# Optimization experiments

Hardware: AMD Instinct MI355X
Metric: run time of the kernel (lower is better)

The kernel has to match this reference:

```python
import jax, jax.numpy as jnp
import numpy as np

N_NODES = 10000
IN_CH = 128
OUT_CH = 128
N_EDGES = 320000


def setup_inputs() -> dict:
    key = jax.random.key(0)
    k1, k2, k3, k4 = jax.random.split(key, 4)
    x = jax.random.normal(k1, (N_NODES, IN_CH), dtype=jnp.float32)
    edge_index = jax.random.randint(k2, (N_EDGES, 2), 0, N_NODES, dtype=jnp.int64)
    # Linear weights (torch stores [out, in]); scale like kaiming-uniform-ish
    w = jax.random.normal(k3, (OUT_CH, IN_CH), dtype=jnp.float32) / np.sqrt(IN_CH)
    b = jax.random.normal(k4, (OUT_CH, IN_CH), dtype=jnp.float32) / np.sqrt(IN_CH)
    return {"x": x, "edge_index": edge_index, "w": w, "b": b}


def reference(x, edge_index, w, b):
    n = x.shape[0]
    # Each edge (i, j) contributes x[j] to node i and x[i] to node j (undirected).
    src = jnp.concatenate([edge_index[:, 1], edge_index[:, 0]])  # feature source
    dst = jnp.concatenate([edge_index[:, 0], edge_index[:, 1]])  # aggregation target
    # segment-sum of gathered neighbor features -> [n, in_ch]
    agg_sum = jax.ops.segment_sum(x[src], dst, num_segments=n)
    deg = jax.ops.segment_sum(jnp.ones_like(dst, dtype=x.dtype), dst, num_segments=n)
    # mean with zero fallback for isolated nodes (original uses zeros vector)
    agg = jnp.where(deg[:, None] > 0, agg_sum / jnp.maximum(deg, 1.0)[:, None], 0.0)
    # out = ReLU(agg @ w^T + x @ b^T)
    return jax.nn.relu(agg @ w.T + x @ b.T)
```

## Files before the change

kernel.cpp:

```cpp
#include <hip/hip_runtime.h>

#define N_NODES 10000
#define CH 128
#define N_EDGES 320000
#define CAP 128
#define CSTR 16


__device__ __forceinline__ unsigned short f2bf(float f) {
    unsigned u = __float_as_uint(f);
    return (unsigned short)((u + 0x7FFFu + ((u >> 16) & 1u)) >> 16);
}
__device__ __forceinline__ float bf2f(unsigned short h) {
    return __uint_as_float(((unsigned)h) << 16);
}

__global__ __launch_bounds__(256) void fill_kernel(const int* __restrict__ ei,
                                                   int* __restrict__ cursor,
                                                   unsigned short* __restrict__ adj)
{
    const int t = blockIdx.x * blockDim.x + threadIdx.x;
    if (t >= N_EDGES) return;
    const int2 p = ((const int2*)ei)[t];
    if ((unsigned)p.x >= N_NODES || (unsigned)p.y >= N_NODES) return;
    const int s0 = atomicAdd(&cursor[p.x * CSTR], 1);
    const int s1 = atomicAdd(&cursor[p.y * CSTR], 1);
    if (s0 < CAP) adj[(size_t)p.x * CAP + s0] = (unsigned short)p.y;
    if (s1 < CAP) adj[(size_t)p.y * CAP + s1] = (unsigned short)p.x;
}

__global__ __launch_bounds__(256) void gather_kernel(const float* __restrict__ x,
                                                     const int* __restrict__ cursor,
                                                     const unsigned short* __restrict__ adj,
                                                     unsigned short* __restrict__ aggb)
{
    const int wv   = threadIdx.x >> 6;
    const int node = blockIdx.x * 4 + wv;
    const int lane = threadIdx.x & 63;
    const int h    = lane >> 5;
    const int l    = lane & 31;

    const int deg = cursor[node * CSTR];
    const int d   = deg < CAP ? deg : CAP;
    const unsigned short* nb = adj + (size_t)node * CAP;

    float4 acc = {0.f, 0.f, 0.f, 0.f};
    const int nit = (d + 1) >> 1;
#pragma unroll 4
    for (int it = 0; it < nit; ++it) {
        const int idx = 2 * it + h;
        int j = nb[idx];
        j = j < N_NODES ? j : 0;
        const float4 u = ((const float4*)(x + (size_t)j * CH))[l];
        const float m = idx < d ? 1.0f : 0.0f;
        acc.x += m * u.x; acc.y += m * u.y; acc.z += m * u.z; acc.w += m * u.w;
    }
    acc.x += __shfl_xor(acc.x, 32, 64);
    acc.y += __shfl_xor(acc.y, 32, 64);
    acc.z += __shfl_xor(acc.z, 32, 64);
    acc.w += __shfl_xor(acc.w, 32, 64);

    if (h == 0) {
        const float inv = deg > 0 ? 1.0f / (float)deg : 0.0f;
        ushort4 o;
        o.x = f2bf(acc.x * inv);
        o.y = f2bf(acc.y * inv);
        o.z = f2bf(acc.z * inv);
        o.w = f2bf(acc.w * inv);
        ((ushort4*)(aggb + (size_t)node * CH))[l] = o;
    }
}

#define NPB 16
__global__ __launch_bounds__(256) void gemm_relu_kernel(const unsigned short* __restrict__ aggb,
                                                        const float* __restrict__ x,
                                                        const float* __restrict__ w,
                                                        const float* __restrict__ b,
                                                        float* __restrict__ out)
{
    __shared__ float sh_a[NPB * CH];
    __shared__ float sh_x[NPB * CH];
    const int tid   = threadIdx.x;
    const int node0 = blockIdx.x * NPB;

    const ushort4* ag = (const ushort4*)(aggb + (size_t)node0 * CH);
#pragma unroll
    for (int r = 0; r < 2; ++r) {
        const ushort4 q = ag[tid + r * 256];
        const int base = (tid + r * 256) * 4;
        sh_a[base + 0] = bf2f(q.x);
        sh_a[base + 1] = bf2f(q.y);
        sh_a[base + 2] = bf2f(q.z);
        sh_a[base + 3] = bf2f(q.w);
    }
    ((float4*)sh_x)[tid]       = ((const float4*)(x + (size_t)node0 * CH))[tid];
    ((float4*)sh_x)[tid + 256] = ((const float4*)(x + (size_t)node0 * CH))[tid + 256];
    __syncthreads();

    const int o = tid & 127;
    const int g = tid >> 7;
    const float4* wr = (const float4*)(w + (size_t)o * CH);
    const float4* br = (const float4*)(b + (size_t)o * CH);
    const float4* A  = (const float4*)(sh_a + (size_t)(g * 8) * CH);
    const float4* X  = (const float4*)(sh_x + (size_t)(g * 8) * CH);

    float acc[8] = {0.f, 0.f, 0.f, 0.f, 0.f, 0.f, 0.f, 0.f};
#pragma unroll 4
    for (int k = 0; k < CH / 4; ++k) {
        const float4 wv = wr[k];
        const float4 bv = br[k];
#pragma unroll
        for (int n = 0; n < 8; ++n) {
            const float4 a4 = A[n * (CH / 4) + k];
            const float4 x4 = X[n * (CH / 4) + k];
            acc[n] += a4.x * wv.x + a4.y * wv.y + a4.z * wv.z + a4.w * wv.w
                    + x4.x * bv.x + x4.y * bv.y + x4.z * bv.z + x4.w * bv.w;
        }
    }
#pragma unroll
    for (int n = 0; n < 8; ++n) {
        const int node = node0 + g * 8 + n;
        const float v = acc[n];
        out[(size_t)node * CH + o] = v > 0.f ? v : 0.f;
    }
}

extern "C" void kernel_launch(void* const* d_in, const int* in_sizes, int n_in,
                              void* d_out, int out_size, void* d_ws, size_t ws_size,
                              hipStream_t stream)
{
    const float* x  = (const float*)d_in[0];
    const int*   ei = (const int*)d_in[1];
    const float* w  = (const float*)d_in[2];
    const float* b  = (const float*)d_in[3];
    float*       out = (float*)d_out;

    int*            cursor = (int*)d_ws;
    unsigned short* adj    = (unsigned short*)((char*)d_ws + 640000);
    unsigned short* aggb   = (unsigned short*)((char*)d_ws + 3200000);

    hipMemsetAsync(d_ws, 0, (size_t)N_NODES * CSTR * sizeof(int), stream);

    fill_kernel<<<(N_EDGES + 255) / 256, 256, 0, stream>>>(ei, cursor, adj);
    gather_kernel<<<N_NODES / 4, 256, 0, stream>>>(x, cursor, adj, aggb);
    gemm_relu_kernel<<<N_NODES / NPB, 256, 0, stream>>>(aggb, x, w, b, out);
}
```

Before: 140.6 us.

## Fuse gather into GEMM, gather bf16 copy of x, merge conversion into fill

The neighbor gather-mean moves into the GEMM kernel, so the aggregate goes straight to shared memory and the bf16 aggregate round-trip through global memory and one launch disappear. Neighbor features are now read from a bf16 copy of x, which halves gather traffic. That copy is built by extra blocks in the same launch as the adjacency fill. In exchange, the fused kernel has only 625 blocks, each doing 16 serial-ish gathers, which may hurt occupancy and latency hiding, and the input features are rounded to bf16 before summation.

```diff
diff --git a/kernel.cpp b/kernel.cpp
--- a/kernel.cpp
+++ b/kernel.cpp
@@ -5,6 +5,11 @@
 #define N_EDGES 320000
 #define CAP 128
 #define CSTR 16
+
+#define FILL_BLOCKS ((N_EDGES + 255) / 256)
+#define CONV_THREADS (N_NODES * CH / 8)
+#define CONV_BLOCKS ((CONV_THREADS + 255) / 256)
+#define NPB 16
 
 
 __device__ __forceinline__ unsigned short f2bf(float f) {
@@ -15,86 +20,93 @@
     return __uint_as_float(((unsigned)h) << 16);
 }
 
-__global__ __launch_bounds__(256) void fill_kernel(const int* __restrict__ ei,
-                                                   int* __restrict__ cursor,
-                                                   unsigned short* __restrict__ adj)
+__global__ __launch_bounds__(256) void fill_conv_kernel(const int* __restrict__ ei,
+                                                        int* __restrict__ cursor,
+                                                        unsigned short* __restrict__ adj,
+                                                        const float* __restrict__ x,
+                                                        unsigned short* __restrict__ xb)
 {
-    const int t = blockIdx.x * blockDim.x + threadIdx.x;
-    if (t >= N_EDGES) return;
-    const int2 p = ((const int2*)ei)[t];
-    if ((unsigned)p.x >= N_NODES || (unsigned)p.y >= N_NODES) return;
-    const int s0 = atomicAdd(&cursor[p.x * CSTR], 1);
-    const int s1 = atomicAdd(&cursor[p.y * CSTR], 1);
-    if (s0 < CAP) adj[(size_t)p.x * CAP + s0] = (unsigned short)p.y;
-    if (s1 < CAP) adj[(size_t)p.y * CAP + s1] = (unsigned short)p.x;
-}
-
-__global__ __launch_bounds__(256) void gather_kernel(const float* __restrict__ x,
-                                                     const int* __restrict__ cursor,
-                                                     const unsigned short* __restrict__ adj,
-                                                     unsigned short* __restrict__ aggb)
-{
-    const int wv   = threadIdx.x >> 6;
-    const int node = blockIdx.x * 4 + wv;
-    const int lane = threadIdx.x & 63;
-    const int h    = lane >> 5;
-    const int l    = lane & 31;
-
-    const int deg = cursor[node * CSTR];
-    const int d   = deg < CAP ? deg : CAP;
-    const unsigned short* nb = adj + (size_t)node * CAP;
-
-    float4 acc = {0.f, 0.f, 0.f, 0.f};
-    const int nit = (d + 1) >> 1;
-#pragma unroll 4
-    for (int it = 0; it < nit; ++it) {
-        const int idx = 2 * it + h;
-        int j = nb[idx];
-        j = j < N_NODES ? j : 0;
-        const float4 u = ((const float4*)(x + (size_t)j * CH))[l];
-        const float m = idx < d ? 1.0f : 0.0f;
-        acc.x += m * u.x; acc.y += m * u.y; acc.z += m * u.z; acc.w += m * u.w;
-    }
-    acc.x += __shfl_xor(acc.x, 32, 64);
-    acc.y += __shfl_xor(acc.y, 32, 64);
-    acc.z += __shfl_xor(acc.z, 32, 64);
-    acc.w += __shfl_xor(acc.w, 32, 64);
-
-    if (h == 0) {
-        const float inv = deg > 0 ? 1.0f / (float)deg : 0.0f;
-        ushort4 o;
-        o.x = f2bf(acc.x * inv);
-        o.y = f2bf(acc.y * inv);
-        o.z = f2bf(acc.z * inv);
-        o.w = f2bf(acc.w * inv);
-        ((ushort4*)(aggb + (size_t)node * CH))[l] = o;
+    const int bid = blockIdx.x;
+    if (bid < FILL_BLOCKS) {
+        const int t = bid * 256 + threadIdx.x;
+        if (t >= N_EDGES) return;
+        const int2 p = ((const int2*)ei)[t];
+        if ((unsigned)p.x >= N_NODES || (unsigned)p.y >= N_NODES) return;
+        const int s0 = atomicAdd(&cursor[p.x * CSTR], 1);
+        const int s1 = atomicAdd(&cursor[p.y * CSTR], 1);
+        if (s0 < CAP) adj[(size_t)p.x * CAP + s0] = (unsigned short)p.y;
+        if (s1 < CAP) adj[(size_t)p.y * CAP + s1] = (unsigned short)p.x;
+    } else {
+        const int t = (bid - FILL_BLOCKS) * 256 + threadIdx.x;
+        if (t >= CONV_THREADS) return;
+        const float4 a = ((const float4*)x)[t * 2];
+        const float4 c = ((const float4*)x)[t * 2 + 1];
+        ushort4 o0, o1;
+        o0.x = f2bf(a.x); o0.y = f2bf(a.y); o0.z = f2bf(a.z); o0.w = f2bf(a.w);
+        o1.x = f2bf(c.x); o1.y = f2bf(c.y); o1.z = f2bf(c.z); o1.w = f2bf(c.w);
+        ((ushort4*)xb)[t * 2]     = o0;
+        ((ushort4*)xb)[t * 2 + 1] = o1;
     }
 }
 
-#define NPB 16
-__global__ __launch_bounds__(256) void gemm_relu_kernel(const unsigned short* __restrict__ aggb,
-                                                        const float* __restrict__ x,
-                                                        const float* __restrict__ w,
-                                                        const float* __restrict__ b,
-                                                        float* __restrict__ out)
+__global__ __launch_bounds__(256) void gather_gemm_kernel(const float* __restrict__ x,
+                                                          const unsigned short* __restrict__ xb,
+                                                          const int* __restrict__ cursor,
+                                                          const unsigned short* __restrict__ adj,
+                                                          const float* __restrict__ w,
+                                                          const float* __restrict__ b,
+                                                          float* __restrict__ out)
 {
     __shared__ float sh_a[NPB * CH];
     __shared__ float sh_x[NPB * CH];
     const int tid   = threadIdx.x;
     const int node0 = blockIdx.x * NPB;
 
-    const ushort4* ag = (const ushort4*)(aggb + (size_t)node0 * CH);
-#pragma unroll
-    for (int r = 0; r < 2; ++r) {
-        const ushort4 q = ag[tid + r * 256];
-        const int base = (tid + r * 256) * 4;
-        sh_a[base + 0] = bf2f(q.x);
-        sh_a[base + 1] = bf2f(q.y);
-        sh_a[base + 2] = bf2f(q.z);
-        sh_a[base + 3] = bf2f(q.w);
+    const float4 xr0 = ((const float4*)(x + (size_t)node0 * CH))[tid];
+    const float4 xr1 = ((const float4*)(x + (size_t)node0 * CH))[tid + 256];
+
+    const int wv   = tid >> 6;
+    const int lane = tid & 63;
+    const int h    = lane >> 5;
+    const int l    = lane & 31;
+
+    for (int i = 0; i < 4; ++i) {
+        const int nl   = wv * 4 + i;
+        const int node = node0 + nl;
+        const int deg  = cursor[node * CSTR];
+        const int d    = deg < CAP ? deg : CAP;
+        const unsigned short* nb = adj + (size_t)node * CAP;
+
+        float4 acc = {0.f, 0.f, 0.f, 0.f};
+        const int nit = (d + 1) >> 1;
+#pragma unroll 4
+        for (int it = 0; it < nit; ++it) {
+            const int idx = 2 * it + h;
+            int j = nb[idx];
+            j = j < N_NODES ? j : 0;
+            const ushort4 u = ((const ushort4*)(xb + (size_t)j * CH))[l];
+            const float m = idx < d ? 1.0f : 0.0f;
+            acc.x += m * bf2f(u.x);
+            acc.y += m * bf2f(u.y);
+            acc.z += m * bf2f(u.z);
+            acc.w += m * bf2f(u.w);
+        }
+        acc.x += __shfl_xor(acc.x, 32, 64);
+        acc.y += __shfl_xor(acc.y, 32, 64);
+        acc.z += __shfl_xor(acc.z, 32, 64);
+        acc.w += __shfl_xor(acc.w, 32, 64);
+
+        if (h == 0) {
+            const float inv = deg > 0 ? 1.0f / (float)deg : 0.0f;
+            float4 o;
+            o.x = acc.x * inv; o.y = acc.y * inv;
+            o.z = acc.z * inv; o.w = acc.w * inv;
+            ((float4*)(sh_a + (size_t)nl * CH))[l] = o;
+        }
     }
-    ((float4*)sh_x)[tid]       = ((const float4*)(x + (size_t)node0 * CH))[tid];
-    ((float4*)sh_x)[tid + 256] = ((const float4*)(x + (size_t)node0 * CH))[tid + 256];
+
+    ((float4*)sh_x)[tid]       = xr0;
+    ((float4*)sh_x)[tid + 256] = xr1;
     __syncthreads();
 
     const int o = tid & 127;
@@ -107,14 +119,14 @@
     float acc[8] = {0.f, 0.f, 0.f, 0.f, 0.f, 0.f, 0.f, 0.f};
 #pragma unroll 4
     for (int k = 0; k < CH / 4; ++k) {
-        const float4 wv = wr[k];
-        const float4 bv = br[k];
+        const float4 wv4 = wr[k];
+        const float4 bv4 = br[k];
 #pragma unroll
         for (int n = 0; n < 8; ++n) {
             const float4 a4 = A[n * (CH / 4) + k];
             const float4 x4 = X[n * (CH / 4) + k];
-            acc[n] += a4.x * wv.x + a4.y * wv.y + a4.z * wv.z + a4.w * wv.w
-                    + x4.x * bv.x + x4.y * bv.y + x4.z * bv.z + x4.w * bv.w;
+            acc[n] += a4.x * wv4.x + a4.y * wv4.y + a4.z * wv4.z + a4.w * wv4.w
+                    + x4.x * bv4.x + x4.y * bv4.y + x4.z * bv4.z + x4.w * bv4.w;
         }
     }
 #pragma unroll
@@ -137,11 +149,10 @@
 
     int*            cursor = (int*)d_ws;
     unsigned short* adj    = (unsigned short*)((char*)d_ws + 640000);
-    unsigned short* aggb   = (unsigned short*)((char*)d_ws + 3200000);
+    unsigned short* xb16   = (unsigned short*)((char*)d_ws + 3200000);
 
     hipMemsetAsync(d_ws, 0, (size_t)N_NODES * CSTR * sizeof(int), stream);
 
-    fill_kernel<<<(N_EDGES + 255) / 256, 256, 0, stream>>>(ei, cursor, adj);
-    gather_kernel<<<N_NODES / 4, 256, 0, stream>>>(x, cursor, adj, aggb);
-    gemm_relu_kernel<<<N_NODES / NPB, 256, 0, stream>>>(aggb, x, w, b, out);
+    fill_conv_kernel<<<FILL_BLOCKS + CONV_BLOCKS, 256, 0, stream>>>(ei, cursor, adj, x, xb16);
+    gather_gemm_kernel<<<N_NODES / NPB, 256, 0, stream>>>(x, xb16, cursor, adj, w, b, out);
 }
```

Result: no change. 142.2 us (+1.1%).

## Use bf16 MFMA GEMM with hi/lo split and bf16 gather of x

Applied to the files above, without the earlier changes.

Converts x, w and b into bf16 hi/lo pairs in a combined fill/convert/pack kernel. The neighbor gather then reads bf16 x instead of fp32, halving gather traffic. The dense GEMM becomes an MFMA 16x16x32 bf16 kernel over a concatenated K dimension that emulates near-fp32 accuracy with split terms. This removes the scalar FP32 GEMM and cuts gather bandwidth. In exchange it adds extra conversion work and workspace, and the gather of bf16 x loses some precision in the mean.

```diff
diff --git a/kernel.cpp b/kernel.cpp
--- a/kernel.cpp
+++ b/kernel.cpp
@@ -6,6 +6,17 @@
 #define CAP 128
 #define CSTR 16
 
+#define FILL_BLOCKS ((N_EDGES + 255) / 256)
+#define CONV_THREADS (N_NODES * CH / 8)
+#define CONV_BLOCKS ((CONV_THREADS + 255) / 256)
+#define PACK_THREADS (128 * 128)
+#define PACK_BLOCKS (PACK_THREADS / 256)
+#define KSEG 5
+#define WBK (KSEG * CH)
+
+
+typedef __attribute__((ext_vector_type(8))) short short8v;
+typedef __attribute__((ext_vector_type(4))) float floatx4;
 
 __device__ __forceinline__ unsigned short f2bf(float f) {
     unsigned u = __float_as_uint(f);
@@ -15,21 +26,63 @@
     return __uint_as_float(((unsigned)h) << 16);
 }
 
-__global__ __launch_bounds__(256) void fill_kernel(const int* __restrict__ ei,
-                                                   int* __restrict__ cursor,
-                                                   unsigned short* __restrict__ adj)
+__global__ __launch_bounds__(256) void fill_conv_pack_kernel(const int* __restrict__ ei,
+                                                             int* __restrict__ cursor,
+                                                             unsigned short* __restrict__ adj,
+                                                             const float* __restrict__ x,
+                                                             unsigned short* __restrict__ xhi,
+                                                             unsigned short* __restrict__ xlo,
+                                                             const float* __restrict__ w,
+                                                             const float* __restrict__ b,
+                                                             unsigned short* __restrict__ wbt)
 {
-    const int t = blockIdx.x * blockDim.x + threadIdx.x;
-    if (t >= N_EDGES) return;
-    const int2 p = ((const int2*)ei)[t];
-    if ((unsigned)p.x >= N_NODES || (unsigned)p.y >= N_NODES) return;
-    const int s0 = atomicAdd(&cursor[p.x * CSTR], 1);
-    const int s1 = atomicAdd(&cursor[p.y * CSTR], 1);
-    if (s0 < CAP) adj[(size_t)p.x * CAP + s0] = (unsigned short)p.y;
-    if (s1 < CAP) adj[(size_t)p.y * CAP + s1] = (unsigned short)p.x;
+    const int bid = blockIdx.x;
+    if (bid < FILL_BLOCKS) {
+        const int t = bid * 256 + threadIdx.x;
+        if (t >= N_EDGES) return;
+        const int2 p = ((const int2*)ei)[t];
+        if ((unsigned)p.x >= N_NODES || (unsigned)p.y >= N_NODES) return;
+        const int s0 = atomicAdd(&cursor[p.x * CSTR], 1);
+        const int s1 = atomicAdd(&cursor[p.y * CSTR], 1);
+        if (s0 < CAP) adj[(size_t)p.x * CAP + s0] = (unsigned short)p.y;
+        if (s1 < CAP) adj[(size_t)p.y * CAP + s1] = (unsigned short)p.x;
+    } else if (bid < FILL_BLOCKS + CONV_BLOCKS) {
+        const int t = (bid - FILL_BLOCKS) * 256 + threadIdx.x;
+        const float4 a = ((const float4*)x)[t * 2];
+        const float4 c = ((const float4*)x)[t * 2 + 1];
+        ushort4 h0, h1, l0, l1;
+        h0.x = f2bf(a.x); l0.x = f2bf(a.x - bf2f(h0.x));
+        h0.y = f2bf(a.y); l0.y = f2bf(a.y - bf2f(h0.y));
+        h0.z = f2bf(a.z); l0.z = f2bf(a.z - bf2f(h0.z));
+        h0.w = f2bf(a.w); l0.w = f2bf(a.w - bf2f(h0.w));
+        h1.x = f2bf(c.x); l1.x = f2bf(c.x - bf2f(h1.x));
+        h1.y = f2bf(c.y); l1.y = f2bf(c.y - bf2f(h1.y));
+        h1.z = f2bf(c.z); l1.z = f2bf(c.z - bf2f(h1.z));
+        h1.w = f2bf(c.w); l1.w = f2bf(c.w - bf2f(h1.w));
+        ((ushort4*)xhi)[t * 2]     = h0;
+        ((ushort4*)xhi)[t * 2 + 1] = h1;
+        ((ushort4*)xlo)[t * 2]     = l0;
+        ((ushort4*)xlo)[t * 2 + 1] = l1;
+    } else {
+        const int t = (bid - FILL_BLOCKS - CONV_BLOCKS) * 256 + threadIdx.x;
+        const int n = t >> 7;
+        const int k = t & 127;
+        const float wv = w[n * CH + k];
+        const float bv = b[n * CH + k];
+        const unsigned short whi = f2bf(wv);
+        const unsigned short wlo = f2bf(wv - bf2f(whi));
+        const unsigned short bhi = f2bf(bv);
+        const unsigned short blo = f2bf(bv - bf2f(bhi));
+        unsigned short* row = wbt + (size_t)n * WBK;
+        row[k]          = whi;
+        row[CH + k]     = wlo;
+        row[2 * CH + k] = bhi;
+        row[3 * CH + k] = blo;
+        row[4 * CH + k] = bhi;
+    }
 }
 
-__global__ __launch_bounds__(256) void gather_kernel(const float* __restrict__ x,
+__global__ __launch_bounds__(256) void gather_kernel(const unsigned short* __restrict__ xhi,
                                                      const int* __restrict__ cursor,
                                                      const unsigned short* __restrict__ adj,
                                                      unsigned short* __restrict__ aggb)
@@ -51,9 +104,12 @@
         const int idx = 2 * it + h;
         int j = nb[idx];
         j = j < N_NODES ? j : 0;
-        const float4 u = ((const float4*)(x + (size_t)j * CH))[l];
+        const ushort4 u = ((const ushort4*)(xhi + (size_t)j * CH))[l];
         const float m = idx < d ? 1.0f : 0.0f;
-        acc.x += m * u.x; acc.y += m * u.y; acc.z += m * u.z; acc.w += m * u.w;
+        acc.x += m * bf2f(u.x);
+        acc.y += m * bf2f(u.y);
+        acc.z += m * bf2f(u.z);
+        acc.w += m * bf2f(u.w);
     }
     acc.x += __shfl_xor(acc.x, 32, 64);
     acc.y += __shfl_xor(acc.y, 32, 64);
@@ -71,57 +127,48 @@
     }
 }
 
-#define NPB 16
-__global__ __launch_bounds__(256) void gemm_relu_kernel(const unsigned short* __restrict__ aggb,
-                                                        const float* __restrict__ x,
-                                                        const float* __restrict__ w,
-                                                        const float* __restrict__ b,
+__global__ __launch_bounds__(256) void mfma_gemm_kernel(const unsigned short* __restrict__ aggb,
+                                                        const unsigned short* __restrict__ xhi,
+                                                        const unsigned short* __restrict__ xlo,
+                                                        const unsigned short* __restrict__ wbt,
                                                         float* __restrict__ out)
 {
-    __shared__ float sh_a[NPB * CH];
-    __shared__ float sh_x[NPB * CH];
-    const int tid   = threadIdx.x;
-    const int node0 = blockIdx.x * NPB;
+    const int wv    = threadIdx.x >> 6;
+    const int lane  = threadIdx.x & 63;
+    const int W     = blockIdx.x * 4 + wv;
+    const int mtile = W >> 2;
+    const int n0    = (W & 3) * 32;
+    const int r     = lane & 15;
+    const int q     = lane >> 4;
+    const int arow  = mtile * 16 + r;
 
-    const ushort4* ag = (const ushort4*)(aggb + (size_t)node0 * CH);
+    floatx4 acc0 = {0.f, 0.f, 0.f, 0.f};
+    floatx4 acc1 = {0.f, 0.f, 0.f, 0.f};
+
 #pragma unroll
-    for (int r = 0; r < 2; ++r) {
-        const ushort4 q = ag[tid + r * 256];
-        const int base = (tid + r * 256) * 4;
-        sh_a[base + 0] = bf2f(q.x);
-        sh_a[base + 1] = bf2f(q.y);
-        sh_a[base + 2] = bf2f(q.z);
-        sh_a[base + 3] = bf2f(q.w);
-    }
-    ((float4*)sh_x)[tid]       = ((const float4*)(x + (size_t)node0 * CH))[tid];
-    ((float4*)sh_x)[tid + 256] = ((const float4*)(x + (size_t)node0 * CH))[tid + 256];
-    __syncthreads();
-
-    const int o = tid & 127;
-    const int g = tid >> 7;
-    const float4* wr = (const float4*)(w + (size_t)o * CH);
-    const float4* br = (const float4*)(b + (size_t)o * CH);
-    const float4* A  = (const float4*)(sh_a + (size_t)(g * 8) * CH);
-    const float4* X  = (const float4*)(sh_x + (size_t)(g * 8) * CH);
-
-    float acc[8] = {0.f, 0.f, 0.f, 0.f, 0.f, 0.f, 0.f, 0.f};
-#pragma unroll 4
-    for (int k = 0; k < CH / 4; ++k) {
-        const float4 wv = wr[k];
-        const float4 bv = br[k];
+    for (int seg = 0; seg < KSEG; ++seg) {
+        const unsigned short* A = (seg < 2) ? aggb : ((seg < 4) ? xhi : xlo);
+        const int wk = seg * CH;
 #pragma unroll
-        for (int n = 0; n < 8; ++n) {
-            const float4 a4 = A[n * (CH / 4) + k];
-            const float4 x4 = X[n * (CH / 4) + k];
-            acc[n] += a4.x * wv.x + a4.y * wv.y + a4.z * wv.z + a4.w * wv.w
-                    + x4.x * bv.x + x4.y * bv.y + x4.z * bv.z + x4.w * bv.w;
+        for (int ks = 0; ks < 4; ++ks) {
+            const int k0 = ks * 32 + q * 8;
+            const short8v af  = *(const short8v*)(A + (size_t)arow * CH + k0);
+            const short8v bf0 = *(const short8v*)(wbt + (size_t)(n0 + r) * WBK + wk + k0);
+            const short8v bf1 = *(const short8v*)(wbt + (size_t)(n0 + 16 + r) * WBK + wk + k0);
+            acc0 = __builtin_amdgcn_mfma_f32_16x16x32_bf16(af, bf0, acc0, 0, 0, 0);
+            acc1 = __builtin_amdgcn_mfma_f32_16x16x32_bf16(af, bf1, acc1, 0, 0, 0);
         }
     }
+
+    const int mbase = mtile * 16 + q * 4;
 #pragma unroll
-    for (int n = 0; n < 8; ++n) {
-        const int node = node0 + g * 8 + n;
-        const float v = acc[n];
-        out[(size_t)node * CH + o] = v > 0.f ? v : 0.f;
+    for (int rr = 0; rr < 4; ++rr) {
+        float v0 = acc0[rr];
+        float v1 = acc1[rr];
+        v0 = v0 > 0.f ? v0 : 0.f;
+        v1 = v1 > 0.f ? v1 : 0.f;
+        out[(size_t)(mbase + rr) * CH + n0 + r]      = v0;
+        out[(size_t)(mbase + rr) * CH + n0 + 16 + r] = v1;
     }
 }
 
@@ -137,11 +184,15 @@
 
     int*            cursor = (int*)d_ws;
     unsigned short* adj    = (unsigned short*)((char*)d_ws + 640000);
-    unsigned short* aggb   = (unsigned short*)((char*)d_ws + 3200000);
+    unsigned short* xhi    = (unsigned short*)((char*)d_ws + 3200000);
+    unsigned short* xlo    = (unsigned short*)((char*)d_ws + 5760000);
+    unsigned short* aggb   = (unsigned short*)((char*)d_ws + 8320000);
+    unsigned short* wbt    = (unsigned short*)((char*)d_ws + 10880000);
 
     hipMemsetAsync(d_ws, 0, (size_t)N_NODES * CSTR * sizeof(int), stream);
 
-    fill_kernel<<<(N_EDGES + 255) / 256, 256, 0, stream>>>(ei, cursor, adj);
-    gather_kernel<<<N_NODES / 4, 256, 0, stream>>>(x, cursor, adj, aggb);
-    gemm_relu_kernel<<<N_NODES / NPB, 256, 0, stream>>>(aggb, x, w, b, out);
+    fill_conv_pack_kernel<<<FILL_BLOCKS + CONV_BLOCKS + PACK_BLOCKS, 256, 0, stream>>>(
+        ei, cursor, adj, x, xhi, xlo, w, b, wbt);
+    gather_kernel<<<N_NODES / 4, 256, 0, stream>>>(xhi, cursor, adj, aggb);
+    mfma_gemm_kernel<<<625, 256, 0, stream>>>(aggb, xhi, xlo, wbt, out);
 }
```

Measured after the change: 131.6 us. -6.4%, faster.
